# Performance work log

Measured on AMD Instinct MI355X. Metric: run time of the kernel, lower is better.

Reference implementation:

```python
import jax, jax.numpy as jnp
import numpy as np

B, T, C, H, E, K = 4, 2048, 512, 2048, 8, 2


def setup_inputs() -> dict:
    key = jax.random.key(0)
    ks = jax.random.split(key, 7)
    s_r = 1.0 / np.sqrt(C)
    s_h = 1.0 / np.sqrt(H)
    return {
        "x": jax.random.normal(ks[0], (B, T, C), dtype=jnp.float32),
        "Wr": jax.random.uniform(ks[1], (C, E), jnp.float32, -s_r, s_r),
        "br": jax.random.uniform(ks[2], (E,), jnp.float32, -s_r, s_r),
        "W1": jax.random.uniform(ks[3], (E, C, H), jnp.float32, -s_r, s_r),
        "b1": jax.random.uniform(ks[4], (E, H), jnp.float32, -s_r, s_r),
        "W2": jax.random.uniform(ks[5], (E, H, C), jnp.float32, -s_h, s_h),
        "b2": jax.random.uniform(ks[6], (E, C), jnp.float32, -s_h, s_h),
    }


def reference(x, Wr, br, W1, b1, W2, b2):
    # Router logits [B,T,E]
    logits = jnp.einsum("btc,ce->bte", x, Wr) + br
    topk_vals, topk_idx = jax.lax.top_k(logits, K)  # [B,T,K]
    scores = jax.nn.softmax(topk_vals, axis=-1)  # softmax over the K selected
    # Combine weights per expert: gate[b,t,e] = sum_k scores[b,t,k]*(idx==e)
    onehot = jax.nn.one_hot(topk_idx, E, dtype=x.dtype)  # [B,T,K,E]
    gate = jnp.einsum("btk,btke->bte", scores, onehot)  # [B,T,E]
    # Dense-masked expert MLPs (tokens not routed to e have gate==0)
    h = jax.nn.relu(jnp.einsum("btc,ech->bteh", x, W1) + b1)  # [B,T,E,H]
    y = jnp.einsum("bteh,ehc->btec", h, W2) + b2  # [B,T,E,C]
    out = jnp.einsum("btec,bte->btc", y, gate)  # weighted combine
    return logits, topk_idx, out
```

## Files before the change

### kernel.cpp

```cpp
#include <hip/hip_runtime.h>
#include <hip/hip_bf16.h>

#define NTOK 8192
#define NASN 16384
#define C_ 512
#define H_ 2048
#define E_ 8
#define NCH 128
#define CHTOK 64
#define MAXT 136

typedef __bf16 bf16x8 __attribute__((ext_vector_type(8)));
typedef float f32x4 __attribute__((ext_vector_type(4)));

#define WS_COUNTS 0
#define WS_BASE   4096
#define WS_OFFS   8192
#define WS_T1S    8448
#define WS_INFO   8704
#define WS_TOKL   (WS_INFO + NTOK*16)
#define WS_GATE   (WS_TOKL + NASN*4)
#define WS_SLOTS  (WS_GATE + NASN*4)
#define WS_XG     (WS_SLOTS + NTOK*8)
#define WS_W1B    (WS_XG + (size_t)NASN*C_*2)
#define WS_W2B    (WS_W1B + (size_t)E_*H_*C_*2)
#define WS_HS     (WS_W2B + (size_t)E_*H_*C_*2)
#define WS_YS     WS_XG

__device__ __forceinline__ unsigned int f2bf(float f) {
  __hip_bfloat16 h = __float2bfloat16(f);
  return (unsigned int)*(unsigned short*)&h;
}

__device__ __forceinline__ void g2l16(const unsigned short* g, unsigned short* l) {
  __builtin_amdgcn_global_load_lds(
      (const __attribute__((address_space(1))) unsigned int*)g,
      (__attribute__((address_space(3))) unsigned int*)l, 16, 0, 0);
}

__global__ __launch_bounds__(256) void k_router(
    const float* __restrict__ x, const float* __restrict__ Wr,
    const float* __restrict__ br, float* __restrict__ out_logits,
    float* __restrict__ out_idx, int4* __restrict__ info,
    int* __restrict__ counts)
{
  int t = blockIdx.x * 4 + (threadIdx.x >> 6);
  int lane = threadIdx.x & 63;
  const float4* xr = (const float4*)(x + (size_t)t * C_);
  float4 x0 = xr[lane*2], x1 = xr[lane*2+1];
  float xs[8] = {x0.x,x0.y,x0.z,x0.w,x1.x,x1.y,x1.z,x1.w};
  float acc[8] = {0,0,0,0,0,0,0,0};
  #pragma unroll
  for (int j = 0; j < 8; j++) {
    const float4* w = (const float4*)(Wr + (size_t)(lane*8+j) * E_);
    float4 w0 = w[0], w1 = w[1];
    float we[8] = {w0.x,w0.y,w0.z,w0.w,w1.x,w1.y,w1.z,w1.w};
    #pragma unroll
    for (int e = 0; e < 8; e++) acc[e] += xs[j] * we[e];
  }
  #pragma unroll
  for (int off = 1; off < 64; off <<= 1) {
    #pragma unroll
    for (int e = 0; e < 8; e++) acc[e] += __shfl_xor(acc[e], off, 64);
  }
  #pragma unroll
  for (int e = 0; e < 8; e++) acc[e] += br[e];
  if (lane == 0) {
    #pragma unroll
    for (int e = 0; e < 8; e++) out_logits[t*8 + e] = acc[e];
    int i0 = 0; float v0 = acc[0];
    #pragma unroll
    for (int e = 1; e < 8; e++) if (acc[e] > v0) { v0 = acc[e]; i0 = e; }
    int i1 = -1; float v1 = -1e30f;
    #pragma unroll
    for (int e = 0; e < 8; e++) if (e != i0 && acc[e] > v1) { v1 = acc[e]; i1 = e; }
    float d = expf(v1 - v0);
    float s1 = d / (1.0f + d);
    float s0 = 1.0f - s1;
    out_idx[t*2]     = (float)i0;
    out_idx[t*2 + 1] = (float)i1;
    info[t] = make_int4(i0, i1, __float_as_int(s0), __float_as_int(s1));
    int ch = t >> 6;
    atomicAdd(&counts[ch*8 + i0], 1);
    atomicAdd(&counts[ch*8 + i1], 1);
  }
}

__global__ __launch_bounds__(256) void k_prefix(
    const int* __restrict__ counts, int* __restrict__ base,
    int* __restrict__ offs, int* __restrict__ t1s)
{
  __shared__ int lc[NCH*8];
  __shared__ int tot[8];
  __shared__ int off_s[9];
  int tid = threadIdx.x;
  for (int i = tid; i < NCH*8; i += 256) lc[i] = counts[i];
  __syncthreads();
  if (tid < 8) {
    int run = 0;
    for (int c = 0; c < NCH; c++) { int v = lc[c*8+tid]; lc[c*8+tid] = run; run += v; }
    tot[tid] = run;
  }
  __syncthreads();
  if (tid == 0) {
    int o = 0, t = 0;
    off_s[0] = 0; offs[0] = 0; t1s[0] = 0;
    for (int e = 0; e < 8; e++) {
      o += tot[e];
      off_s[e+1] = o; offs[e+1] = o;
      t += (tot[e] + 127) >> 7;
      t1s[e+1] = t;
    }
  }
  __syncthreads();
  for (int i = tid; i < NCH*8; i += 256) base[i] = off_s[i & 7] + lc[i];
}

__global__ __launch_bounds__(64) void k_scatter(
    const int4* __restrict__ info, const int* __restrict__ base,
    int* __restrict__ tokl, float* __restrict__ gate, int2* __restrict__ slots2)
{
  __shared__ int cur[8];
  int c = blockIdx.x, tid = threadIdx.x;
  if (tid < 8) cur[tid] = base[c*8 + tid];
  __syncthreads();
  int t = c * CHTOK + tid;
  int4 nfo = info[t];
  int r0 = atomicAdd(&cur[nfo.x], 1);
  int r1 = atomicAdd(&cur[nfo.y], 1);
  tokl[r0] = t; gate[r0] = __int_as_float(nfo.z);
  tokl[r1] = t; gate[r1] = __int_as_float(nfo.w);
  slots2[t] = make_int2(r0, r1);
}

__global__ __launch_bounds__(256) void k_gather(
    const float* __restrict__ x, const int* __restrict__ tokl,
    unsigned short* __restrict__ Xg)
{
  int slot = blockIdx.x * 4 + (threadIdx.x >> 6);
  int lane = threadIdx.x & 63;
  int t = tokl[slot];
  const float4* xr = (const float4*)(x + (size_t)t * C_);
  float4 x0 = xr[lane*2], x1 = xr[lane*2+1];
  uint4 pk;
  pk.x = f2bf(x0.x) | (f2bf(x0.y) << 16);
  pk.y = f2bf(x0.z) | (f2bf(x0.w) << 16);
  pk.z = f2bf(x1.x) | (f2bf(x1.y) << 16);
  pk.w = f2bf(x1.z) | (f2bf(x1.w) << 16);
  *(uint4*)(Xg + (size_t)slot * C_ + lane*8) = pk;
}

__global__ __launch_bounds__(256) void k_transpose(
    const float* __restrict__ in, unsigned short* __restrict__ outp, int R, int S)
{
  __shared__ float tile[32][33];
  size_t zo = (size_t)blockIdx.z * R * S;
  in += zo; outp += zo;
  int s0 = blockIdx.x * 32, r0 = blockIdx.y * 32;
  int tx = threadIdx.x, ty = threadIdx.y;
  #pragma unroll
  for (int i = 0; i < 4; i++)
    tile[ty + i*8][tx] = in[(size_t)(r0 + ty + i*8) * S + s0 + tx];
  __syncthreads();
  #pragma unroll
  for (int i = 0; i < 4; i++)
    outp[(size_t)(s0 + ty + i*8) * R + r0 + tx] = f2bf(tile[tx][ty + i*8]);
}

__global__ __launch_bounds__(256) void k_gemm1(
    const unsigned short* __restrict__ Xg, const unsigned short* __restrict__ W1b,
    const float* __restrict__ b1, unsigned short* __restrict__ Hs,
    const int* __restrict__ offs, const int* __restrict__ t1s)
{
  __shared__ __align__(16) unsigned short AB[2*128*64];
  unsigned short* Al = AB;
  unsigned short* Bl = AB + 128*64;
  int mt = blockIdx.y;
  if (mt >= t1s[8]) return;
  int e = 0;
  #pragma unroll
  for (int i = 0; i < 7; i++) if (mt >= t1s[e+1]) e++;
  int row0 = offs[e] + (mt - t1s[e]) * 128;
  int rowEnd = offs[e+1];
  int n0 = blockIdx.x * 128;
  int tid = threadIdx.x, lane = tid & 63, w = tid >> 6;
  int wm = (w & 1) * 64, wn = (w >> 1) * 64;
  int quad = lane >> 4, l16 = lane & 15;
  const f32x4 zero = {0.f, 0.f, 0.f, 0.f};
  f32x4 acc[4][4];
  #pragma unroll
  for (int i = 0; i < 4; i++)
    #pragma unroll
    for (int j = 0; j < 4; j++) acc[i][j] = zero;
  const unsigned short* Bsrc = W1b + ((size_t)e * H_ + n0) * C_;

  const unsigned short* ga[4]; const unsigned short* gb[4];
  unsigned short* la[4]; unsigned short* lb[4];
  #pragma unroll
  for (int j = 0; j < 4; j++) {
    int L = (w*4 + j)*64 + lane;
    int row = L >> 3;
    int cc = (L & 7) ^ (row & 7);
    int gr = row0 + row; gr = gr < NASN-1 ? gr : NASN-1;
    ga[j] = Xg + (size_t)gr * C_ + cc*8;
    gb[j] = Bsrc + (size_t)row * C_ + cc*8;
    la[j] = Al + (w*4 + j)*512;
    lb[j] = Bl + (w*4 + j)*512;
  }
  int r7 = l16 & 7;

  for (int kk = 0; kk < C_; kk += 64) {
    #pragma unroll
    for (int j = 0; j < 4; j++) {
      g2l16(ga[j] + kk, la[j]);
      g2l16(gb[j] + kk, lb[j]);
    }
    __syncthreads();
    #pragma unroll
    for (int ks4 = 0; ks4 < 8; ks4 += 4) {
      int chunk = (ks4 + quad) ^ r7;
      bf16x8 af[4], bfr[4];
      #pragma unroll
      for (int i = 0; i < 4; i++)
        af[i] = *(const bf16x8*)&Al[(wm + i*16 + l16)*64 + chunk*8];
      #pragma unroll
      for (int j = 0; j < 4; j++)
        bfr[j] = *(const bf16x8*)&Bl[(wn + j*16 + l16)*64 + chunk*8];
      #pragma unroll
      for (int i = 0; i < 4; i++)
        #pragma unroll
        for (int j = 0; j < 4; j++)
          acc[i][j] = __builtin_amdgcn_mfma_f32_16x16x32_bf16(af[i], bfr[j], acc[i][j], 0, 0, 0);
    }
    __syncthreads();
  }

  unsigned short* Lt = AB + w*4096;
  #pragma unroll
  for (int j = 0; j < 4; j++) {
    int n = n0 + wn + j*16 + l16;
    float bias = b1[e * H_ + n];
    #pragma unroll
    for (int i = 0; i < 4; i++)
      #pragma unroll
      for (int r = 0; r < 4; r++) {
        float v = acc[i][j][r] + bias;
        Lt[(i*16 + quad*4 + r)*64 + j*16 + l16] = (unsigned short)f2bf(v > 0.f ? v : 0.f);
      }
  }
  #pragma unroll
  for (int it = 0; it < 8; it++) {
    int rloc = it*8 + (lane >> 3);
    int m = row0 + wm + rloc;
    uint4 vv = *(uint4*)&Lt[rloc*64 + (lane & 7)*8];
    if (m < rowEnd)
      *(uint4*)(Hs + (size_t)m * H_ + n0 + wn + (lane & 7)*8) = vv;
  }
}

__global__ __launch_bounds__(256) void k_gemm2(
    const unsigned short* __restrict__ Hs, const unsigned short* __restrict__ W2b,
    const float* __restrict__ b2, float* __restrict__ Ys,
    const int* __restrict__ offs, const int* __restrict__ t1s)
{
  __shared__ __align__(16) unsigned short AB[2*128*64];
  unsigned short* Al = AB;
  unsigned short* Bl = AB + 128*64;
  int mt = blockIdx.y;
  if (mt >= t1s[8]) return;
  int e = 0;
  #pragma unroll
  for (int i = 0; i < 7; i++) if (mt >= t1s[e+1]) e++;
  int row0 = offs[e] + (mt - t1s[e]) * 128;
  int rowEnd = offs[e+1];
  int n0 = blockIdx.x * 128;
  int tid = threadIdx.x, lane = tid & 63, w = tid >> 6;
  int wm = (w & 1) * 64, wn = (w >> 1) * 64;
  int quad = lane >> 4, l16 = lane & 15;
  const f32x4 zero = {0.f, 0.f, 0.f, 0.f};
  f32x4 acc[4][4];
  #pragma unroll
  for (int i = 0; i < 4; i++)
    #pragma unroll
    for (int j = 0; j < 4; j++) acc[i][j] = zero;
  const unsigned short* Bsrc = W2b + ((size_t)e * C_ + n0) * H_;

  const unsigned short* ga[4]; const unsigned short* gb[4];
  unsigned short* la[4]; unsigned short* lb[4];
  #pragma unroll
  for (int j = 0; j < 4; j++) {
    int L = (w*4 + j)*64 + lane;
    int row = L >> 3;
    int cc = (L & 7) ^ (row & 7);
    int gr = row0 + row; gr = gr < NASN-1 ? gr : NASN-1;
    ga[j] = Hs + (size_t)gr * H_ + cc*8;
    gb[j] = Bsrc + (size_t)row * H_ + cc*8;
    la[j] = Al + (w*4 + j)*512;
    lb[j] = Bl + (w*4 + j)*512;
  }
  int r7 = l16 & 7;

  for (int kk = 0; kk < H_; kk += 64) {
    #pragma unroll
    for (int j = 0; j < 4; j++) {
      g2l16(ga[j] + kk, la[j]);
      g2l16(gb[j] + kk, lb[j]);
    }
    __syncthreads();
    #pragma unroll
    for (int ks4 = 0; ks4 < 8; ks4 += 4) {
      int chunk = (ks4 + quad) ^ r7;
      bf16x8 af[4], bfr[4];
      #pragma unroll
      for (int i = 0; i < 4; i++)
        af[i] = *(const bf16x8*)&Al[(wm + i*16 + l16)*64 + chunk*8];
      #pragma unroll
      for (int j = 0; j < 4; j++)
        bfr[j] = *(const bf16x8*)&Bl[(wn + j*16 + l16)*64 + chunk*8];
      #pragma unroll
      for (int i = 0; i < 4; i++)
        #pragma unroll
        for (int j = 0; j < 4; j++)
          acc[i][j] = __builtin_amdgcn_mfma_f32_16x16x32_bf16(af[i], bfr[j], acc[i][j], 0, 0, 0);
    }
    __syncthreads();
  }

  float* Lt = (float*)AB + w*2048;
  #pragma unroll
  for (int h = 0; h < 2; h++) {
    #pragma unroll
    for (int j = 0; j < 4; j++) {
      int n = n0 + wn + j*16 + l16;
      float bias = b2[e * C_ + n];
      #pragma unroll
      for (int ii = 0; ii < 2; ii++) {
        int i = h*2 + ii;
        #pragma unroll
        for (int r = 0; r < 4; r++)
          Lt[(ii*16 + quad*4 + r)*64 + j*16 + l16] = acc[i][j][r] + bias;
      }
    }
    #pragma unroll
    for (int it = 0; it < 8; it++) {
      int rloc = it*4 + (lane >> 4);
      int m = row0 + wm + h*32 + rloc;
      float4 vv = *(float4*)&Lt[rloc*64 + (lane & 15)*4];
      if (m < rowEnd)
        *(float4*)(Ys + (size_t)m * C_ + n0 + wn + (lane & 15)*4) = vv;
    }
  }
}

__global__ __launch_bounds__(256) void k_combine(
    const float* __restrict__ Ys, const int4* __restrict__ info,
    const int2* __restrict__ slots2, float* __restrict__ outp)
{
  int t = blockIdx.x * 4 + (threadIdx.x >> 6);
  int lane = threadIdx.x & 63;
  int4 nfo = info[t];
  int2 ss = slots2[t];
  float g0 = __int_as_float(nfo.z), g1 = __int_as_float(nfo.w);
  const float4* ya = (const float4*)(Ys + (size_t)ss.x * C_);
  const float4* yb = (const float4*)(Ys + (size_t)ss.y * C_);
  float4* o = (float4*)(outp + (size_t)t * C_);
  #pragma unroll
  for (int i = 0; i < 2; i++) {
    float4 a = ya[lane*2 + i], b = yb[lane*2 + i];
    float4 r;
    r.x = g0*a.x + g1*b.x; r.y = g0*a.y + g1*b.y;
    r.z = g0*a.z + g1*b.z; r.w = g0*a.w + g1*b.w;
    o[lane*2 + i] = r;
  }
}

extern "C" void kernel_launch(void* const* d_in, const int* in_sizes, int n_in,
                              void* d_out, int out_size, void* d_ws, size_t ws_size,
                              hipStream_t stream)
{
  const float* x  = (const float*)d_in[0];
  const float* Wr = (const float*)d_in[1];
  const float* br = (const float*)d_in[2];
  const float* W1 = (const float*)d_in[3];
  const float* b1 = (const float*)d_in[4];
  const float* W2 = (const float*)d_in[5];
  const float* b2 = (const float*)d_in[6];
  float* out = (float*)d_out;
  char* ws = (char*)d_ws;

  int*  counts = (int*)(ws + WS_COUNTS);
  int*  base   = (int*)(ws + WS_BASE);
  int*  offs   = (int*)(ws + WS_OFFS);
  int*  t1s    = (int*)(ws + WS_T1S);
  int4* info   = (int4*)(ws + WS_INFO);
  int*  tokl   = (int*)(ws + WS_TOKL);
  float* gate  = (float*)(ws + WS_GATE);
  int2* slots2 = (int2*)(ws + WS_SLOTS);
  unsigned short* Xg  = (unsigned short*)(ws + WS_XG);
  unsigned short* W1b = (unsigned short*)(ws + WS_W1B);
  unsigned short* W2b = (unsigned short*)(ws + WS_W2B);
  unsigned short* Hs  = (unsigned short*)(ws + WS_HS);
  float* Ys = (float*)(ws + WS_YS);

  hipMemsetAsync(counts, 0, NCH*8*sizeof(int), stream);

  k_transpose<<<dim3(H_/32, C_/32, E_), dim3(32, 8), 0, stream>>>(W1, W1b, C_, H_);
  k_transpose<<<dim3(C_/32, H_/32, E_), dim3(32, 8), 0, stream>>>(W2, W2b, H_, C_);
  k_router<<<NTOK/4, 256, 0, stream>>>(x, Wr, br, out, out + 65536, info, counts);
  k_prefix<<<1, 256, 0, stream>>>(counts, base, offs, t1s);
  k_scatter<<<NCH, 64, 0, stream>>>(info, base, tokl, gate, slots2);
  k_gather<<<NASN/4, 256, 0, stream>>>(x, tokl, Xg);
  k_gemm1<<<dim3(16, MAXT), 256, 0, stream>>>(Xg, W1b, b1, Hs, offs, t1s);
  k_gemm2<<<dim3(4, MAXT), 256, 0, stream>>>(Hs, W2b, b2, Ys, offs, t1s);
  k_combine<<<NTOK/4, 256, 0, stream>>>(Ys, info, slots2, out + 81920);
}
```

Measured before the change: 303.2 us.

## Fuse gather into router and GEMM1, split-K GEMM2 with bf16 output

The router kernel now writes a bf16 copy of x, and GEMM1 reads token rows indirectly through tokl, so the separate gather kernel and the unused gate array are gone. Both GEMMs use a 1D grid with a grouped tile order (8 M-tiles per N sweep) meant to improve L2 reuse of the weights. GEMM2 runs 512 threads with an in-block split-K over H, reduces the two halves through LDS, and stores Y as bf16, which halves the Y traffic into the combine kernel. The cost is lower precision in the combine stage and extra LDS and sync work in GEMM2.

Measured after the change: 305.7 us. Within noise of the previous version (+0.8%).

```diff
diff --git a/kernel.cpp b/kernel.cpp
--- a/kernel.cpp
+++ b/kernel.cpp
@@ -19,17 +19,19 @@
 #define WS_T1S    8448
 #define WS_INFO   8704
 #define WS_TOKL   (WS_INFO + NTOK*16)
-#define WS_GATE   (WS_TOKL + NASN*4)
-#define WS_SLOTS  (WS_GATE + NASN*4)
-#define WS_XG     (WS_SLOTS + NTOK*8)
-#define WS_W1B    (WS_XG + (size_t)NASN*C_*2)
+#define WS_SLOTS  (WS_TOKL + NASN*4)
+#define WS_XBF    (WS_SLOTS + NTOK*8)
+#define WS_W1B    (WS_XBF + (size_t)NTOK*C_*2)
 #define WS_W2B    (WS_W1B + (size_t)E_*H_*C_*2)
 #define WS_HS     (WS_W2B + (size_t)E_*H_*C_*2)
-#define WS_YS     WS_XG
+#define WS_YS     WS_XBF
 
 __device__ __forceinline__ unsigned int f2bf(float f) {
   __hip_bfloat16 h = __float2bfloat16(f);
   return (unsigned int)*(unsigned short*)&h;
+}
+__device__ __forceinline__ float bf2f(unsigned int u) {
+  return __int_as_float((u & 0xffffu) << 16);
 }
 
 __device__ __forceinline__ void g2l16(const unsigned short* g, unsigned short* l) {
@@ -42,12 +44,19 @@
     const float* __restrict__ x, const float* __restrict__ Wr,
     const float* __restrict__ br, float* __restrict__ out_logits,
     float* __restrict__ out_idx, int4* __restrict__ info,
-    int* __restrict__ counts)
+    int* __restrict__ counts, unsigned short* __restrict__ Xbf)
 {
   int t = blockIdx.x * 4 + (threadIdx.x >> 6);
   int lane = threadIdx.x & 63;
   const float4* xr = (const float4*)(x + (size_t)t * C_);
   float4 x0 = xr[lane*2], x1 = xr[lane*2+1];
+  uint4 pk;
+  pk.x = f2bf(x0.x) | (f2bf(x0.y) << 16);
+  pk.y = f2bf(x0.z) | (f2bf(x0.w) << 16);
+  pk.z = f2bf(x1.x) | (f2bf(x1.y) << 16);
+  pk.w = f2bf(x1.z) | (f2bf(x1.w) << 16);
+  *(uint4*)(Xbf + (size_t)t * C_ + lane*8) = pk;
+
   float xs[8] = {x0.x,x0.y,x0.z,x0.w,x1.x,x1.y,x1.z,x1.w};
   float acc[8] = {0,0,0,0,0,0,0,0};
   #pragma unroll
@@ -118,7 +127,7 @@
 
 __global__ __launch_bounds__(64) void k_scatter(
     const int4* __restrict__ info, const int* __restrict__ base,
-    int* __restrict__ tokl, float* __restrict__ gate, int2* __restrict__ slots2)
+    int* __restrict__ tokl, int2* __restrict__ slots2)
 {
   __shared__ int cur[8];
   int c = blockIdx.x, tid = threadIdx.x;
@@ -128,26 +137,9 @@
   int4 nfo = info[t];
   int r0 = atomicAdd(&cur[nfo.x], 1);
   int r1 = atomicAdd(&cur[nfo.y], 1);
-  tokl[r0] = t; gate[r0] = __int_as_float(nfo.z);
-  tokl[r1] = t; gate[r1] = __int_as_float(nfo.w);
+  tokl[r0] = t;
+  tokl[r1] = t;
   slots2[t] = make_int2(r0, r1);
-}
-
-__global__ __launch_bounds__(256) void k_gather(
-    const float* __restrict__ x, const int* __restrict__ tokl,
-    unsigned short* __restrict__ Xg)
-{
-  int slot = blockIdx.x * 4 + (threadIdx.x >> 6);
-  int lane = threadIdx.x & 63;
-  int t = tokl[slot];
-  const float4* xr = (const float4*)(x + (size_t)t * C_);
-  float4 x0 = xr[lane*2], x1 = xr[lane*2+1];
-  uint4 pk;
-  pk.x = f2bf(x0.x) | (f2bf(x0.y) << 16);
-  pk.y = f2bf(x0.z) | (f2bf(x0.w) << 16);
-  pk.z = f2bf(x1.x) | (f2bf(x1.y) << 16);
-  pk.w = f2bf(x1.z) | (f2bf(x1.w) << 16);
-  *(uint4*)(Xg + (size_t)slot * C_ + lane*8) = pk;
 }
 
 __global__ __launch_bounds__(256) void k_transpose(
@@ -168,21 +160,24 @@
 }
 
 __global__ __launch_bounds__(256) void k_gemm1(
-    const unsigned short* __restrict__ Xg, const unsigned short* __restrict__ W1b,
+    const unsigned short* __restrict__ Xbf, const int* __restrict__ tokl,
+    const unsigned short* __restrict__ W1b,
     const float* __restrict__ b1, unsigned short* __restrict__ Hs,
     const int* __restrict__ offs, const int* __restrict__ t1s)
 {
   __shared__ __align__(16) unsigned short AB[2*128*64];
   unsigned short* Al = AB;
   unsigned short* Bl = AB + 128*64;
-  int mt = blockIdx.y;
+  int b = blockIdx.x;
+  int mo = b >> 7, rr = b & 127;
+  int n0 = (rr >> 3) * 128;
+  int mt = mo*8 + (rr & 7);
   if (mt >= t1s[8]) return;
   int e = 0;
   #pragma unroll
   for (int i = 0; i < 7; i++) if (mt >= t1s[e+1]) e++;
   int row0 = offs[e] + (mt - t1s[e]) * 128;
   int rowEnd = offs[e+1];
-  int n0 = blockIdx.x * 128;
   int tid = threadIdx.x, lane = tid & 63, w = tid >> 6;
   int wm = (w & 1) * 64, wn = (w >> 1) * 64;
   int quad = lane >> 4, l16 = lane & 15;
@@ -202,7 +197,8 @@
     int row = L >> 3;
     int cc = (L & 7) ^ (row & 7);
     int gr = row0 + row; gr = gr < NASN-1 ? gr : NASN-1;
-    ga[j] = Xg + (size_t)gr * C_ + cc*8;
+    int trow = tokl[gr];
+    ga[j] = Xbf + (size_t)trow * C_ + cc*8;
     gb[j] = Bsrc + (size_t)row * C_ + cc*8;
     la[j] = Al + (w*4 + j)*512;
     lb[j] = Bl + (w*4 + j)*512;
@@ -258,24 +254,25 @@
   }
 }
 
-__global__ __launch_bounds__(256) void k_gemm2(
+__global__ __launch_bounds__(512) void k_gemm2(
     const unsigned short* __restrict__ Hs, const unsigned short* __restrict__ W2b,
-    const float* __restrict__ b2, float* __restrict__ Ys,
+    const float* __restrict__ b2, unsigned short* __restrict__ Ys,
     const int* __restrict__ offs, const int* __restrict__ t1s)
 {
-  __shared__ __align__(16) unsigned short AB[2*128*64];
-  unsigned short* Al = AB;
-  unsigned short* Bl = AB + 128*64;
-  int mt = blockIdx.y;
+  __shared__ __align__(16) unsigned short AB[2*2*128*64];
+  int b = blockIdx.x;
+  int g = b >> 5, rr = b & 31;
+  int n0 = (rr >> 3) * 128;
+  int mt = g*8 + (rr & 7);
   if (mt >= t1s[8]) return;
   int e = 0;
   #pragma unroll
   for (int i = 0; i < 7; i++) if (mt >= t1s[e+1]) e++;
   int row0 = offs[e] + (mt - t1s[e]) * 128;
   int rowEnd = offs[e+1];
-  int n0 = blockIdx.x * 128;
   int tid = threadIdx.x, lane = tid & 63, w = tid >> 6;
-  int wm = (w & 1) * 64, wn = (w >> 1) * 64;
+  int wq = w >> 1, kh = w & 1;
+  int wm = (wq & 1) * 64, wn = (wq >> 1) * 64;
   int quad = lane >> 4, l16 = lane & 15;
   const f32x4 zero = {0.f, 0.f, 0.f, 0.f};
   f32x4 acc[4][4];
@@ -289,18 +286,20 @@
   unsigned short* la[4]; unsigned short* lb[4];
   #pragma unroll
   for (int j = 0; j < 4; j++) {
-    int L = (w*4 + j)*64 + lane;
+    int L = (wq*4 + j)*64 + lane;
     int row = L >> 3;
     int cc = (L & 7) ^ (row & 7);
     int gr = row0 + row; gr = gr < NASN-1 ? gr : NASN-1;
-    ga[j] = Hs + (size_t)gr * H_ + cc*8;
-    gb[j] = Bsrc + (size_t)row * H_ + cc*8;
-    la[j] = Al + (w*4 + j)*512;
-    lb[j] = Bl + (w*4 + j)*512;
+    ga[j] = Hs + (size_t)gr * H_ + kh*1024 + cc*8;
+    gb[j] = Bsrc + (size_t)row * H_ + kh*1024 + cc*8;
+    la[j] = AB + kh*16384 + (wq*4 + j)*512;
+    lb[j] = AB + kh*16384 + 8192 + (wq*4 + j)*512;
   }
   int r7 = l16 & 7;
-
-  for (int kk = 0; kk < H_; kk += 64) {
+  const unsigned short* Ap = AB + kh*16384;
+  const unsigned short* Bp = AB + kh*16384 + 8192;
+
+  for (int kk = 0; kk < 1024; kk += 64) {
     #pragma unroll
     for (int j = 0; j < 4; j++) {
       g2l16(ga[j] + kk, la[j]);
@@ -313,10 +312,10 @@
       bf16x8 af[4], bfr[4];
       #pragma unroll
       for (int i = 0; i < 4; i++)
-        af[i] = *(const bf16x8*)&Al[(wm + i*16 + l16)*64 + chunk*8];
+        af[i] = *(const bf16x8*)&Ap[(wm + i*16 + l16)*64 + chunk*8];
       #pragma unroll
       for (int j = 0; j < 4; j++)
-        bfr[j] = *(const bf16x8*)&Bl[(wn + j*16 + l16)*64 + chunk*8];
+        bfr[j] = *(const bf16x8*)&Bp[(wn + j*16 + l16)*64 + chunk*8];
       #pragma unroll
       for (int i = 0; i < 4; i++)
         #pragma unroll
@@ -326,34 +325,56 @@
     __syncthreads();
   }
 
-  float* Lt = (float*)AB + w*2048;
-  #pragma unroll
-  for (int h = 0; h < 2; h++) {
+  float* X = (float*)AB;
+  if (kh == 1) {
+    #pragma unroll
+    for (int i = 0; i < 4; i++)
+      #pragma unroll
+      for (int j = 0; j < 4; j++) {
+        int c = j*16 + l16;
+        int slot = (i*4 + quad) ^ (c & 15);
+        *(f32x4*)&X[wq*4096 + c*64 + slot*4] = acc[i][j];
+      }
+  }
+  __syncthreads();
+  if (kh == 0) {
     #pragma unroll
     for (int j = 0; j < 4; j++) {
-      int n = n0 + wn + j*16 + l16;
-      float bias = b2[e * C_ + n];
-      #pragma unroll
-      for (int ii = 0; ii < 2; ii++) {
-        int i = h*2 + ii;
+      int c = j*16 + l16;
+      float bias = b2[e * C_ + n0 + wn + c];
+      #pragma unroll
+      for (int i = 0; i < 4; i++) {
+        int slot = (i*4 + quad) ^ (c & 15);
+        f32x4 p = *(const f32x4*)&X[wq*4096 + c*64 + slot*4];
+        #pragma unroll
+        for (int r = 0; r < 4; r++) acc[i][j][r] += p[r] + bias;
+      }
+    }
+  }
+  __syncthreads();
+  if (kh == 0) {
+    unsigned short* Lt = AB + wq*4096;
+    #pragma unroll
+    for (int j = 0; j < 4; j++)
+      #pragma unroll
+      for (int i = 0; i < 4; i++)
         #pragma unroll
         for (int r = 0; r < 4; r++)
-          Lt[(ii*16 + quad*4 + r)*64 + j*16 + l16] = acc[i][j][r] + bias;
-      }
-    }
+          Lt[(i*16 + quad*4 + r)*64 + j*16 + l16] =
+              (unsigned short)f2bf(acc[i][j][r]);
     #pragma unroll
     for (int it = 0; it < 8; it++) {
-      int rloc = it*4 + (lane >> 4);
-      int m = row0 + wm + h*32 + rloc;
-      float4 vv = *(float4*)&Lt[rloc*64 + (lane & 15)*4];
+      int rloc = it*8 + (lane >> 3);
+      int m = row0 + wm + rloc;
+      uint4 vv = *(uint4*)&Lt[rloc*64 + (lane & 7)*8];
       if (m < rowEnd)
-        *(float4*)(Ys + (size_t)m * C_ + n0 + wn + (lane & 15)*4) = vv;
+        *(uint4*)(Ys + (size_t)m * C_ + n0 + wn + (lane & 7)*8) = vv;
     }
   }
 }
 
 __global__ __launch_bounds__(256) void k_combine(
-    const float* __restrict__ Ys, const int4* __restrict__ info,
+    const unsigned short* __restrict__ Ys, const int4* __restrict__ info,
     const int2* __restrict__ slots2, float* __restrict__ outp)
 {
   int t = blockIdx.x * 4 + (threadIdx.x >> 6);
@@ -361,17 +382,27 @@
   int4 nfo = info[t];
   int2 ss = slots2[t];
   float g0 = __int_as_float(nfo.z), g1 = __int_as_float(nfo.w);
-  const float4* ya = (const float4*)(Ys + (size_t)ss.x * C_);
-  const float4* yb = (const float4*)(Ys + (size_t)ss.y * C_);
-  float4* o = (float4*)(outp + (size_t)t * C_);
-  #pragma unroll
-  for (int i = 0; i < 2; i++) {
-    float4 a = ya[lane*2 + i], b = yb[lane*2 + i];
-    float4 r;
-    r.x = g0*a.x + g1*b.x; r.y = g0*a.y + g1*b.y;
-    r.z = g0*a.z + g1*b.z; r.w = g0*a.w + g1*b.w;
-    o[lane*2 + i] = r;
-  }
+  uint4 a = *(const uint4*)(Ys + (size_t)ss.x * C_ + lane*8);
+  uint4 bb = *(const uint4*)(Ys + (size_t)ss.y * C_ + lane*8);
+  unsigned int au[4] = {a.x, a.y, a.z, a.w};
+  unsigned int bu[4] = {bb.x, bb.y, bb.z, bb.w};
+  float4 o0, o1;
+  float* op = &o0.x;
+  #pragma unroll
+  for (int q = 0; q < 4; q++) {
+    op[q*2 - (q>=2?0:0)] = 0;
+  }
+  float vals[8];
+  #pragma unroll
+  for (int q = 0; q < 4; q++) {
+    vals[q*2]   = g0*bf2f(au[q])        + g1*bf2f(bu[q]);
+    vals[q*2+1] = g0*bf2f(au[q] >> 16)  + g1*bf2f(bu[q] >> 16);
+  }
+  o0.x = vals[0]; o0.y = vals[1]; o0.z = vals[2]; o0.w = vals[3];
+  o1.x = vals[4]; o1.y = vals[5]; o1.z = vals[6]; o1.w = vals[7];
+  float4* o = (float4*)(outp + (size_t)t * C_ + lane*8);
+  o[0] = o0;
+  o[1] = o1;
 }
 
 extern "C" void kernel_launch(void* const* d_in, const int* in_sizes, int n_in,
@@ -394,23 +425,21 @@
   int*  t1s    = (int*)(ws + WS_T1S);
   int4* info   = (int4*)(ws + WS_INFO);
   int*  tokl   = (int*)(ws + WS_TOKL);
-  float* gate  = (float*)(ws + WS_GATE);
   int2* slots2 = (int2*)(ws + WS_SLOTS);
-  unsigned short* Xg  = (unsigned short*)(ws + WS_XG);
+  unsigned short* Xbf = (unsigned short*)(ws + WS_XBF);
   unsigned short* W1b = (unsigned short*)(ws + WS_W1B);
   unsigned short* W2b = (unsigned short*)(ws + WS_W2B);
   unsigned short* Hs  = (unsigned short*)(ws + WS_HS);
-  float* Ys = (float*)(ws + WS_YS);
+  unsigned short* Ys  = (unsigned short*)(ws + WS_YS);
 
   hipMemsetAsync(counts, 0, NCH*8*sizeof(int), stream);
 
   k_transpose<<<dim3(H_/32, C_/32, E_), dim3(32, 8), 0, stream>>>(W1, W1b, C_, H_);
   k_transpose<<<dim3(C_/32, H_/32, E_), dim3(32, 8), 0, stream>>>(W2, W2b, H_, C_);
-  k_router<<<NTOK/4, 256, 0, stream>>>(x, Wr, br, out, out + 65536, info, counts);
+  k_router<<<NTOK/4, 256, 0, stream>>>(x, Wr, br, out, out + 65536, info, counts, Xbf);
   k_prefix<<<1, 256, 0, stream>>>(counts, base, offs, t1s);
-  k_scatter<<<NCH, 64, 0, stream>>>(info, base, tokl, gate, slots2);
-  k_gather<<<NASN/4, 256, 0, stream>>>(x, tokl, Xg);
-  k_gemm1<<<dim3(16, MAXT), 256, 0, stream>>>(Xg, W1b, b1, Hs, offs, t1s);
-  k_gemm2<<<dim3(4, MAXT), 256, 0, stream>>>(Hs, W2b, b2, Ys, offs, t1s);
+  k_scatter<<<NCH, 64, 0, stream>>>(info, base, tokl, slots2);
+  k_gemm1<<<17*128, 256, 0, stream>>>(Xbf, tokl, W1b, b1, Hs, offs, t1s);
+  k_gemm2<<<17*32, 512, 0, stream>>>(Hs, W2b, b2, Ys, offs, t1s);
   k_combine<<<NTOK/4, 256, 0, stream>>>(Ys, info, slots2, out + 81920);
 }
```
